# Kernel tuning notes

Hardware: AMD Instinct MI355X
Metric: run time of the kernel (lower is better)

## Reference

```python
import jax, jax.numpy as jnp
import numpy as np

B, S, H, F, E, K = 4, 2048, 512, 2048, 8, 2


def setup_inputs() -> dict:
    key = jax.random.key(0)
    ks = jax.random.split(key, 6)
    s_h = 1.0 / np.sqrt(H)
    s_f = 1.0 / np.sqrt(F)
    return {
        "x": jax.random.normal(ks[0], (B, S, H), dtype=jnp.float32),
        "router_w": jax.random.uniform(ks[1], (E, H), jnp.float32, -s_h, s_h),
        "fc1_w": jax.random.uniform(ks[2], (E, F, H), jnp.float32, -s_h, s_h),
        "fc1_b": jax.random.uniform(ks[3], (E, F), jnp.float32, -s_h, s_h),
        "fc2_w": jax.random.uniform(ks[4], (E, H, F), jnp.float32, -s_f, s_f),
        "fc2_b": jax.random.uniform(ks[5], (E, H), jnp.float32, -s_f, s_f),
    }


def reference(x, router_w, fc1_w, fc1_b, fc2_w, fc2_b):
    # Router: Linear (no bias), softmax over experts, top-k, renormalize.
    logits = jnp.einsum("bsh,eh->bse", x, router_w)           # [B,S,E]
    probs = jax.nn.softmax(logits, axis=-1)                    # [B,S,E]
    topk_p, topk_i = jax.lax.top_k(probs, K)                   # [B,S,K]
    topk_p = topk_p / (jnp.sum(topk_p, axis=-1, keepdims=True) + 1e-9)

    # Original loop runs every expert FFN on all tokens and masks;
    # mathematically identical: dense per-expert FFN, then gather+combine.
    h1 = jnp.einsum("bsh,efh->bsef", x, fc1_w) + fc1_b         # [B,S,E,F]
    a = jax.nn.gelu(h1, approximate=False)                     # exact erf GELU (torch nn.GELU default)
    y = jnp.einsum("bsef,ehf->bseh", a, fc2_w) + fc2_b         # [B,S,E,H]

    sel = jnp.take_along_axis(y, topk_i[..., None], axis=2)    # [B,S,K,H]
    output = jnp.sum(topk_p[..., None] * sel, axis=2)          # [B,S,H]
    return output, probs, topk_i
```

## Files before the change

### kernel.cpp

```cpp
#include <hip/hip_runtime.h>

#define T_TOKENS 8192
#define HD 512
#define FD 2048
#define NE 8
#define CAP 8192
#define CSTRIDE 32

#define BM 128
#define BN 128
#define BK 32

typedef __attribute__((ext_vector_type(8))) short short8;
typedef __attribute__((ext_vector_type(4))) float f32x4;

__device__ __forceinline__ ushort f2bf(float f) {
  union { float f; unsigned u; } v; v.f = f;
  unsigned u = v.u;
  return (ushort)((u + 0x7fffu + ((u >> 16) & 1u)) >> 16);
}

__device__ __forceinline__ void gld16(const void* g, void* l) {
  __builtin_amdgcn_global_load_lds(
      (const __attribute__((address_space(1))) void*)g,
      (__attribute__((address_space(3))) void*)l, 16, 0, 0);
}

__global__ void cvt_bf16(const float4* __restrict__ src, ushort4* __restrict__ dst, int n4) {
  int i = blockIdx.x * blockDim.x + threadIdx.x;
  int st = gridDim.x * blockDim.x;
  for (; i < n4; i += st) {
    float4 v = src[i];
    ushort4 o;
    o.x = f2bf(v.x); o.y = f2bf(v.y); o.z = f2bf(v.z); o.w = f2bf(v.w);
    dst[i] = o;
  }
}

#define TPW 16
__global__ void router_kernel(const float* __restrict__ x, const float* __restrict__ rw,
                              float* __restrict__ probs_out, float* __restrict__ topk_out,
                              int* __restrict__ counts, int* __restrict__ bucket_tok,
                              float* __restrict__ bucket_w, int4* __restrict__ tok_info) {
  __shared__ int lcnt[NE];
  __shared__ int lbase[NE];
  __shared__ int ls_e0[64], ls_e1[64], ls_s0[64], ls_s1[64];
  __shared__ float ls_w0[64], ls_w1[64];

  int wave = threadIdx.x >> 6, lane = threadIdx.x & 63;
  if (threadIdx.x < NE) lcnt[threadIdx.x] = 0;
  __syncthreads();

  int tbase = blockIdx.x * 64;
  for (int it = 0; it < TPW; it++) {
    int lt = wave * TPW + it;
    int t = tbase + lt;
    float acc[NE];
#pragma unroll
    for (int e = 0; e < NE; e++) acc[e] = 0.f;
    const float* xr = x + (size_t)t * HD;
    for (int c = 0; c < HD; c += 64) {
      float xv = xr[c + lane];
#pragma unroll
      for (int e = 0; e < NE; e++) acc[e] += xv * rw[e * HD + c + lane];
    }
#pragma unroll
    for (int e = 0; e < NE; e++) {
#pragma unroll
      for (int s = 32; s > 0; s >>= 1) acc[e] += __shfl_xor(acc[e], s, 64);
    }
    if (lane == 0) {
      float m = acc[0];
#pragma unroll
      for (int e = 1; e < NE; e++) m = fmaxf(m, acc[e]);
      float p[NE], s = 0.f;
#pragma unroll
      for (int e = 0; e < NE; e++) { p[e] = expf(acc[e] - m); s += p[e]; }
      float inv = 1.f / s;
#pragma unroll
      for (int e = 0; e < NE; e++) { p[e] *= inv; probs_out[(size_t)t * NE + e] = p[e]; }
      int i0 = 0;
#pragma unroll
      for (int e = 1; e < NE; e++) if (p[e] > p[i0]) i0 = e;
      int i1 = (i0 == 0) ? 1 : 0;
#pragma unroll
      for (int e = 0; e < NE; e++) if (e != i0 && p[e] > p[i1]) i1 = e;
      float r = 1.f / (p[i0] + p[i1] + 1e-9f);
      topk_out[(size_t)t * 2 + 0] = (float)i0;
      topk_out[(size_t)t * 2 + 1] = (float)i1;
      ls_e0[lt] = i0; ls_e1[lt] = i1;
      ls_w0[lt] = p[i0] * r; ls_w1[lt] = p[i1] * r;
      ls_s0[lt] = atomicAdd(&lcnt[i0], 1);
      ls_s1[lt] = atomicAdd(&lcnt[i1], 1);
    }
  }
  __syncthreads();
  if (threadIdx.x < NE)
    lbase[threadIdx.x] = atomicAdd(&counts[threadIdx.x * CSTRIDE], lcnt[threadIdx.x]);
  __syncthreads();
  if (threadIdx.x < 64) {
    int lt = threadIdx.x, t = tbase + lt;
    int e0 = ls_e0[lt], e1 = ls_e1[lt];
    int g0 = lbase[e0] + ls_s0[lt];
    int g1 = lbase[e1] + ls_s1[lt];
    bucket_tok[e0 * CAP + g0] = t; bucket_w[e0 * CAP + g0] = ls_w0[lt];
    bucket_tok[e1 * CAP + g1] = t; bucket_w[e1 * CAP + g1] = ls_w1[lt];
    tok_info[t] = make_int4(e0, e1, g0, g1);
  }
}

__global__ void scan_kernel(const int* __restrict__ counts, int* __restrict__ offsets) {
  if (threadIdx.x == 0) {
    int o = 0;
#pragma unroll
    for (int e = 0; e < NE; e++) { offsets[e] = o; o += counts[e * CSTRIDE]; }
  }
}

template <bool IS_FC1>
__global__ __launch_bounds__(256, 2)
void ffn_gemm(const ushort* __restrict__ Ab, const ushort* __restrict__ Bw,
              const float* __restrict__ bias, const int* __restrict__ counts,
              const int* __restrict__ offsets, const int* __restrict__ bucket_tok,
              const float* __restrict__ bucket_w, ushort* __restrict__ Aout,
              float* __restrict__ Yout, int KD, int ND) {
  int e = blockIdx.z;
  int cnt = counts[e * CSTRIDE];
  int m0 = blockIdx.y * BM;
  if (m0 >= cnt) return;
  int n0 = blockIdx.x * BN;
  int off = offsets[e];

  __shared__ alignas(16) ushort smem[10240];
  ushort* As = smem;
  ushort* Bs = smem + BM * BK;

  int tid = threadIdx.x;
  int wid = tid >> 6, lid = tid & 63;
  int wm = wid >> 1, wn = wid & 1;
  int q = lid >> 4, l16 = lid & 15;

  int crow = tid >> 2;
  int cseg = (tid & 3) * 8;

  int mr0 = min(m0 + crow, cnt - 1);
  int mr1 = min(m0 + crow + 64, cnt - 1);
  const ushort *a0, *a1;
  if (IS_FC1) {
    a0 = Ab + (size_t)bucket_tok[e * CAP + mr0] * KD + cseg;
    a1 = Ab + (size_t)bucket_tok[e * CAP + mr1] * KD + cseg;
  } else {
    a0 = Ab + (size_t)(off + mr0) * KD + cseg;
    a1 = Ab + (size_t)(off + mr1) * KD + cseg;
  }
  const ushort* b0 = Bw + ((size_t)e * ND + n0 + crow) * KD + cseg;
  const ushort* b1 = b0 + (size_t)64 * KD;
  ushort* lA0 = As + tid * 8;
  ushort* lA1 = As + (tid + 256) * 8;
  ushort* lB0 = Bs + tid * 8;
  ushort* lB1 = Bs + (tid + 256) * 8;

  f32x4 acc[4][4] = {};

  for (int k0 = 0; k0 < KD; k0 += BK) {
    gld16(a0 + k0, lA0);
    gld16(a1 + k0, lA1);
    gld16(b0 + k0, lB0);
    gld16(b1 + k0, lB1);
    __syncthreads();
    short8 af[4], bfr[4];
#pragma unroll
    for (int i = 0; i < 4; i++)
      af[i] = *(const short8*)&As[(wm * 64 + i * 16 + l16) * BK + q * 8];
#pragma unroll
    for (int j = 0; j < 4; j++)
      bfr[j] = *(const short8*)&Bs[(wn * 64 + j * 16 + l16) * BK + q * 8];
#pragma unroll
    for (int i = 0; i < 4; i++)
#pragma unroll
      for (int j = 0; j < 4; j++)
        acc[i][j] = __builtin_amdgcn_mfma_f32_16x16x32_bf16(af[i], bfr[j], acc[i][j], 0, 0, 0);
    __syncthreads();
  }

  float bcol[4];
#pragma unroll
  for (int j = 0; j < 4; j++)
    bcol[j] = bias[(size_t)e * ND + n0 + wn * 64 + j * 16 + l16];

  if (IS_FC1) {
    ushort* Ct = smem;
#pragma unroll
    for (int i = 0; i < 4; i++) {
      __syncthreads();
#pragma unroll
      for (int j = 0; j < 4; j++)
#pragma unroll
        for (int r = 0; r < 4; r++) {
          float v = acc[i][j][r] + bcol[j];
          float g = 0.5f * v * (1.0f + erff(v * 0.70710678118654752f));
          Ct[(wm * 16 + q * 4 + r) * 136 + wn * 64 + j * 16 + l16] = f2bf(g);
        }
      __syncthreads();
#pragma unroll
      for (int u = 0; u < 2; u++) {
        int c = tid + u * 256;
        int ml = c >> 4, cc = c & 15;
        int gm = m0 + (ml >> 4) * 64 + i * 16 + (ml & 15);
        if (gm < cnt)
          *(uint4*)&Aout[(size_t)(off + gm) * ND + n0 + cc * 8] =
              *(const uint4*)&Ct[ml * 136 + cc * 8];
      }
    }
  } else {
    float* Ct = (float*)smem;
#pragma unroll
    for (int i = 0; i < 4; i++) {
      __syncthreads();
#pragma unroll
      for (int r = 0; r < 4; r++) {
        int gm = m0 + wm * 64 + i * 16 + q * 4 + r;
        float wgt = bucket_w[e * CAP + min(gm, cnt - 1)];
#pragma unroll
        for (int j = 0; j < 4; j++)
          Ct[(wm * 16 + q * 4 + r) * 132 + wn * 64 + j * 16 + l16] = wgt * (acc[i][j][r] + bcol[j]);
      }
      __syncthreads();
#pragma unroll
      for (int u = 0; u < 4; u++) {
        int c = tid + u * 256;
        int ml = c >> 5, cc = c & 31;
        int gm = m0 + (ml >> 4) * 64 + i * 16 + (ml & 15);
        if (gm < cnt)
          *(float4*)&Yout[(size_t)(off + gm) * ND + n0 + cc * 4] =
              *(const float4*)&Ct[ml * 132 + cc * 4];
      }
    }
  }
}

__global__ void combine_kernel(const float4* __restrict__ Y, const int4* __restrict__ tok_info,
                               const int* __restrict__ offsets, float4* __restrict__ out) {
  int t = blockIdx.x;
  int4 ti = tok_info[t];
  int g0 = offsets[ti.x] + ti.z;
  int g1 = offsets[ti.y] + ti.w;
  int i = threadIdx.x;
  float4 a = Y[(size_t)g0 * (HD / 4) + i];
  float4 b = Y[(size_t)g1 * (HD / 4) + i];
  out[(size_t)t * (HD / 4) + i] = make_float4(a.x + b.x, a.y + b.y, a.z + b.z, a.w + b.w);
}

extern "C" void kernel_launch(void* const* d_in, const int* in_sizes, int n_in,
                              void* d_out, int out_size, void* d_ws, size_t ws_size,
                              hipStream_t stream) {
  const float* x    = (const float*)d_in[0];
  const float* rw   = (const float*)d_in[1];
  const float* fc1w = (const float*)d_in[2];
  const float* fc1b = (const float*)d_in[3];
  const float* fc2w = (const float*)d_in[4];
  const float* fc2b = (const float*)d_in[5];

  float* out   = (float*)d_out;
  float* probs = out + (size_t)T_TOKENS * HD;
  float* topk  = probs + (size_t)T_TOKENS * NE;

  char* p = (char*)d_ws;
  auto carve = [&](size_t bytes) { char* r = p; p += (bytes + 255) & ~(size_t)255; return r; };
  int*    counts     = (int*)carve(NE * CSTRIDE * sizeof(int));
  int*    offsets    = (int*)carve(NE * sizeof(int));
  int*    bucket_tok = (int*)carve((size_t)NE * CAP * sizeof(int));
  float*  bucket_w   = (float*)carve((size_t)NE * CAP * sizeof(float));
  int4*   tok_info   = (int4*)carve((size_t)T_TOKENS * sizeof(int4));
  ushort* xb   = (ushort*)carve((size_t)T_TOKENS * HD * 2);
  ushort* w1b  = (ushort*)carve((size_t)NE * FD * HD * 2);
  ushort* w2b  = (ushort*)carve((size_t)NE * HD * FD * 2);
  ushort* Abuf = (ushort*)carve((size_t)T_TOKENS * 2 * FD * 2);
  float*  Y    = (float*)carve((size_t)T_TOKENS * 2 * HD * 4);

  hipMemsetAsync(counts, 0, NE * CSTRIDE * sizeof(int), stream);
  cvt_bf16<<<2048, 256, 0, stream>>>((const float4*)x, (ushort4*)xb, T_TOKENS * HD / 4);
  cvt_bf16<<<2048, 256, 0, stream>>>((const float4*)fc1w, (ushort4*)w1b, NE * FD * HD / 4);
  cvt_bf16<<<2048, 256, 0, stream>>>((const float4*)fc2w, (ushort4*)w2b, NE * HD * FD / 4);
  router_kernel<<<T_TOKENS / 64, 256, 0, stream>>>(x, rw, probs, topk, counts, bucket_tok,
                                                   bucket_w, tok_info);
  scan_kernel<<<1, 64, 0, stream>>>(counts, offsets);
  ffn_gemm<true><<<dim3(FD / BN, CAP / BM, NE), 256, 0, stream>>>(
      xb, w1b, fc1b, counts, offsets, bucket_tok, bucket_w, Abuf, nullptr, HD, FD);
  ffn_gemm<false><<<dim3(HD / BN, CAP / BM, NE), 256, 0, stream>>>(
      Abuf, w2b, fc2b, counts, offsets, bucket_tok, bucket_w, nullptr, Y, FD, HD);
  combine_kernel<<<T_TOKENS, 128, 0, stream>>>((const float4*)Y, tok_info, offsets, (float4*)out);
}
```

Baseline: 339.1 us.

## Fuse fp32-to-bf16 weight conversion into FFN GEMM tile loads

```diff
diff --git a/kernel.cpp b/kernel.cpp
--- a/kernel.cpp
+++ b/kernel.cpp
@@ -8,8 +8,6 @@
 #define CSTRIDE 32
 
 #define BM 128
-#define BN 128
-#define BK 32
 
 typedef __attribute__((ext_vector_type(8))) short short8;
 typedef __attribute__((ext_vector_type(4))) float f32x4;
@@ -20,10 +18,9 @@
   return (ushort)((u + 0x7fffu + ((u >> 16) & 1u)) >> 16);
 }
 
-__device__ __forceinline__ void gld16(const void* g, void* l) {
-  __builtin_amdgcn_global_load_lds(
-      (const __attribute__((address_space(1))) void*)g,
-      (__attribute__((address_space(3))) void*)l, 16, 0, 0);
+__device__ __forceinline__ unsigned pack_trunc(float lo, float hi) {
+  union { float f; unsigned u; } a, b; a.f = lo; b.f = hi;
+  return __builtin_amdgcn_perm(b.u, a.u, 0x07060302);
 }
 
 __global__ void cvt_bf16(const float4* __restrict__ src, ushort4* __restrict__ dst, int n4) {
@@ -117,84 +114,112 @@
   }
 }
 
-template <bool IS_FC1>
+template <int BN_, bool IS_FC1>
 __global__ __launch_bounds__(256, 2)
-void ffn_gemm(const ushort* __restrict__ Ab, const ushort* __restrict__ Bw,
+void ffn_gemm(const ushort* __restrict__ Ab, const float* __restrict__ Bw,
               const float* __restrict__ bias, const int* __restrict__ counts,
               const int* __restrict__ offsets, const int* __restrict__ bucket_tok,
               const float* __restrict__ bucket_w, ushort* __restrict__ Aout,
               float* __restrict__ Yout, int KD, int ND) {
+  constexpr int JW = BN_ / 32;
+  constexpr int BCH_PT = BN_ / 32;
+
   int e = blockIdx.z;
   int cnt = counts[e * CSTRIDE];
   int m0 = blockIdx.y * BM;
   if (m0 >= cnt) return;
-  int n0 = blockIdx.x * BN;
+  int n0 = blockIdx.x * BN_;
   int off = offsets[e];
 
-  __shared__ alignas(16) ushort smem[10240];
-  ushort* As = smem;
-  ushort* Bs = smem + BM * BK;
+  __shared__ alignas(16) ushort As[8 * BM * 8];
+  __shared__ alignas(16) ushort Bs[8 * BN_ * 8];
 
   int tid = threadIdx.x;
   int wid = tid >> 6, lid = tid & 63;
   int wm = wid >> 1, wn = wid & 1;
   int q = lid >> 4, l16 = lid & 15;
 
-  int crow = tid >> 2;
-  int cseg = (tid & 3) * 8;
-
-  int mr0 = min(m0 + crow, cnt - 1);
-  int mr1 = min(m0 + crow + 64, cnt - 1);
-  const ushort *a0, *a1;
+  int kc = tid & 7;
+  int rbase = tid >> 3;
+
+  const ushort* aptr[4];
+  int aoff[4];
+#pragma unroll
+  for (int u = 0; u < 4; u++) {
+    int m = rbase + u * 32;
+    int mr = min(m0 + m, cnt - 1);
+    int row = IS_FC1 ? bucket_tok[e * CAP + mr] : (off + mr);
+    aptr[u] = Ab + (size_t)row * KD + kc * 8;
+    aoff[u] = (kc * BM + (m ^ kc)) * 8;
+  }
+  const float* bptr[BCH_PT];
+  int boff[BCH_PT];
+#pragma unroll
+  for (int u = 0; u < BCH_PT; u++) {
+    int n = rbase + u * 32;
+    bptr[u] = Bw + ((size_t)e * ND + n0 + n) * KD + kc * 8;
+    boff[u] = (kc * BN_ + (n ^ kc)) * 8;
+  }
+
+  f32x4 acc[4][JW] = {};
+
+  for (int k0 = 0; k0 < KD; k0 += 64) {
+    uint4 av[4];
+#pragma unroll
+    for (int u = 0; u < 4; u++) av[u] = *(const uint4*)(aptr[u] + k0);
+    float4 bv0[BCH_PT], bv1[BCH_PT];
+#pragma unroll
+    for (int u = 0; u < BCH_PT; u++) {
+      bv0[u] = *(const float4*)(bptr[u] + k0);
+      bv1[u] = *(const float4*)(bptr[u] + k0 + 4);
+    }
+#pragma unroll
+    for (int u = 0; u < 4; u++) *(uint4*)&As[aoff[u]] = av[u];
+#pragma unroll
+    for (int u = 0; u < BCH_PT; u++) {
+      uint4 o;
+      o.x = pack_trunc(bv0[u].x, bv0[u].y);
+      o.y = pack_trunc(bv0[u].z, bv0[u].w);
+      o.z = pack_trunc(bv1[u].x, bv1[u].y);
+      o.w = pack_trunc(bv1[u].z, bv1[u].w);
+      *(uint4*)&Bs[boff[u]] = o;
+    }
+    __syncthreads();
+#pragma unroll
+    for (int t = 0; t < 2; t++) {
+      int kcc = t * 4 + q;
+      short8 af[4], bfr[JW];
+#pragma unroll
+      for (int i = 0; i < 4; i++) {
+        int m = wm * 64 + i * 16 + l16;
+        af[i] = *(const short8*)&As[((kcc * BM) + (m ^ kcc)) * 8];
+      }
+#pragma unroll
+      for (int j = 0; j < JW; j++) {
+        int n = wn * (16 * JW) + j * 16 + l16;
+        bfr[j] = *(const short8*)&Bs[((kcc * BN_) + (n ^ kcc)) * 8];
+      }
+#pragma unroll
+      for (int i = 0; i < 4; i++)
+#pragma unroll
+        for (int j = 0; j < JW; j++)
+          acc[i][j] = __builtin_amdgcn_mfma_f32_16x16x32_bf16(af[i], bfr[j], acc[i][j], 0, 0, 0);
+    }
+    __syncthreads();
+  }
+
+  float bcol[JW];
+#pragma unroll
+  for (int j = 0; j < JW; j++)
+    bcol[j] = bias[(size_t)e * ND + n0 + wn * (16 * JW) + j * 16 + l16];
+
   if (IS_FC1) {
-    a0 = Ab + (size_t)bucket_tok[e * CAP + mr0] * KD + cseg;
-    a1 = Ab + (size_t)bucket_tok[e * CAP + mr1] * KD + cseg;
-  } else {
-    a0 = Ab + (size_t)(off + mr0) * KD + cseg;
-    a1 = Ab + (size_t)(off + mr1) * KD + cseg;
-  }
-  const ushort* b0 = Bw + ((size_t)e * ND + n0 + crow) * KD + cseg;
-  const ushort* b1 = b0 + (size_t)64 * KD;
-  ushort* lA0 = As + tid * 8;
-  ushort* lA1 = As + (tid + 256) * 8;
-  ushort* lB0 = Bs + tid * 8;
-  ushort* lB1 = Bs + (tid + 256) * 8;
-
-  f32x4 acc[4][4] = {};
-
-  for (int k0 = 0; k0 < KD; k0 += BK) {
-    gld16(a0 + k0, lA0);
-    gld16(a1 + k0, lA1);
-    gld16(b0 + k0, lB0);
-    gld16(b1 + k0, lB1);
-    __syncthreads();
-    short8 af[4], bfr[4];
-#pragma unroll
-    for (int i = 0; i < 4; i++)
-      af[i] = *(const short8*)&As[(wm * 64 + i * 16 + l16) * BK + q * 8];
-#pragma unroll
-    for (int j = 0; j < 4; j++)
-      bfr[j] = *(const short8*)&Bs[(wn * 64 + j * 16 + l16) * BK + q * 8];
-#pragma unroll
-    for (int i = 0; i < 4; i++)
-#pragma unroll
-      for (int j = 0; j < 4; j++)
-        acc[i][j] = __builtin_amdgcn_mfma_f32_16x16x32_bf16(af[i], bfr[j], acc[i][j], 0, 0, 0);
-    __syncthreads();
-  }
-
-  float bcol[4];
-#pragma unroll
-  for (int j = 0; j < 4; j++)
-    bcol[j] = bias[(size_t)e * ND + n0 + wn * 64 + j * 16 + l16];
-
-  if (IS_FC1) {
-    ushort* Ct = smem;
+    ushort* Ct = As;
 #pragma unroll
     for (int i = 0; i < 4; i++) {
       __syncthreads();
 #pragma unroll
-      for (int j = 0; j < 4; j++)
+      for (int j = 0; j < JW; j++)
 #pragma unroll
         for (int r = 0; r < 4; r++) {
           float v = acc[i][j][r] + bcol[j];
@@ -213,7 +238,7 @@
       }
     }
   } else {
-    float* Ct = (float*)smem;
+    float* Ct = (float*)As;
 #pragma unroll
     for (int i = 0; i < 4; i++) {
       __syncthreads();
@@ -222,18 +247,18 @@
         int gm = m0 + wm * 64 + i * 16 + q * 4 + r;
         float wgt = bucket_w[e * CAP + min(gm, cnt - 1)];
 #pragma unroll
-        for (int j = 0; j < 4; j++)
-          Ct[(wm * 16 + q * 4 + r) * 132 + wn * 64 + j * 16 + l16] = wgt * (acc[i][j][r] + bcol[j]);
+        for (int j = 0; j < JW; j++)
+          Ct[(wm * 16 + q * 4 + r) * 68 + wn * 32 + j * 16 + l16] = wgt * (acc[i][j][r] + bcol[j]);
       }
       __syncthreads();
 #pragma unroll
-      for (int u = 0; u < 4; u++) {
+      for (int u = 0; u < 2; u++) {
         int c = tid + u * 256;
-        int ml = c >> 5, cc = c & 31;
+        int ml = c >> 4, cc = c & 15;
         int gm = m0 + (ml >> 4) * 64 + i * 16 + (ml & 15);
         if (gm < cnt)
           *(float4*)&Yout[(size_t)(off + gm) * ND + n0 + cc * 4] =
-              *(const float4*)&Ct[ml * 132 + cc * 4];
+              *(const float4*)&Ct[ml * 68 + cc * 4];
       }
     }
   }
@@ -273,21 +298,17 @@
   float*  bucket_w   = (float*)carve((size_t)NE * CAP * sizeof(float));
   int4*   tok_info   = (int4*)carve((size_t)T_TOKENS * sizeof(int4));
   ushort* xb   = (ushort*)carve((size_t)T_TOKENS * HD * 2);
-  ushort* w1b  = (ushort*)carve((size_t)NE * FD * HD * 2);
-  ushort* w2b  = (ushort*)carve((size_t)NE * HD * FD * 2);
   ushort* Abuf = (ushort*)carve((size_t)T_TOKENS * 2 * FD * 2);
   float*  Y    = (float*)carve((size_t)T_TOKENS * 2 * HD * 4);
 
   hipMemsetAsync(counts, 0, NE * CSTRIDE * sizeof(int), stream);
   cvt_bf16<<<2048, 256, 0, stream>>>((const float4*)x, (ushort4*)xb, T_TOKENS * HD / 4);
-  cvt_bf16<<<2048, 256, 0, stream>>>((const float4*)fc1w, (ushort4*)w1b, NE * FD * HD / 4);
-  cvt_bf16<<<2048, 256, 0, stream>>>((const float4*)fc2w, (ushort4*)w2b, NE * HD * FD / 4);
   router_kernel<<<T_TOKENS / 64, 256, 0, stream>>>(x, rw, probs, topk, counts, bucket_tok,
                                                    bucket_w, tok_info);
   scan_kernel<<<1, 64, 0, stream>>>(counts, offsets);
-  ffn_gemm<true><<<dim3(FD / BN, CAP / BM, NE), 256, 0, stream>>>(
-      xb, w1b, fc1b, counts, offsets, bucket_tok, bucket_w, Abuf, nullptr, HD, FD);
-  ffn_gemm<false><<<dim3(HD / BN, CAP / BM, NE), 256, 0, stream>>>(
-      Abuf, w2b, fc2b, counts, offsets, bucket_tok, bucket_w, nullptr, Y, FD, HD);
+  ffn_gemm<128, true><<<dim3(FD / 128, CAP / BM, NE), 256, 0, stream>>>(
+      xb, fc1w, fc1b, counts, offsets, bucket_tok, bucket_w, Abuf, nullptr, HD, FD);
+  ffn_gemm<64, false><<<dim3(HD / 64, CAP / BM, NE), 256, 0, stream>>>(
+      Abuf, fc2w, fc2b, counts, offsets, bucket_tok, bucket_w, nullptr, Y, FD, HD);
   combine_kernel<<<T_TOKENS, 128, 0, stream>>>((const float4*)Y, tok_info, offsets, (float4*)out);
 }
```

After: 351.2 us. 3.6% more time.

## Double-buffer LDS tiles with k-chunk-major layout in expert GEMM

Applied to the files above, without the earlier changes.

```diff
diff --git a/kernel.cpp b/kernel.cpp
--- a/kernel.cpp
+++ b/kernel.cpp
@@ -118,7 +118,7 @@
 }
 
 template <bool IS_FC1>
-__global__ __launch_bounds__(256, 2)
+__global__ __launch_bounds__(256, 3)
 void ffn_gemm(const ushort* __restrict__ Ab, const ushort* __restrict__ Bw,
               const float* __restrict__ bias, const int* __restrict__ counts,
               const int* __restrict__ offsets, const int* __restrict__ bucket_tok,
@@ -131,56 +131,59 @@
   int n0 = blockIdx.x * BN;
   int off = offsets[e];
 
-  __shared__ alignas(16) ushort smem[10240];
-  ushort* As = smem;
-  ushort* Bs = smem + BM * BK;
+  __shared__ alignas(16) ushort smem[16384];
 
   int tid = threadIdx.x;
-  int wid = tid >> 6, lid = tid & 63;
+  int wid = tid >> 6, lane = tid & 63;
   int wm = wid >> 1, wn = wid & 1;
-  int q = lid >> 4, l16 = lid & 15;
-
-  int crow = tid >> 2;
-  int cseg = (tid & 3) * 8;
-
-  int mr0 = min(m0 + crow, cnt - 1);
-  int mr1 = min(m0 + crow + 64, cnt - 1);
-  const ushort *a0, *a1;
-  if (IS_FC1) {
-    a0 = Ab + (size_t)bucket_tok[e * CAP + mr0] * KD + cseg;
-    a1 = Ab + (size_t)bucket_tok[e * CAP + mr1] * KD + cseg;
-  } else {
-    a0 = Ab + (size_t)(off + mr0) * KD + cseg;
-    a1 = Ab + (size_t)(off + mr1) * KD + cseg;
-  }
-  const ushort* b0 = Bw + ((size_t)e * ND + n0 + crow) * KD + cseg;
-  const ushort* b1 = b0 + (size_t)64 * KD;
-  ushort* lA0 = As + tid * 8;
-  ushort* lA1 = As + (tid + 256) * 8;
-  ushort* lB0 = Bs + tid * 8;
-  ushort* lB1 = Bs + (tid + 256) * 8;
+  int q = lane >> 4, l16 = lane & 15;
+
+  int srow = tid & 127;
+  int kc0 = tid >> 7;
+  int mr = min(m0 + srow, cnt - 1);
+  int arow = IS_FC1 ? bucket_tok[e * CAP + mr] : (off + mr);
+  const ushort* ag = Ab + (size_t)arow * KD + kc0 * 8;
+  const ushort* bg = Bw + ((size_t)e * ND + n0 + srow) * KD + kc0 * 8;
 
   f32x4 acc[4][4] = {};
-
-  for (int k0 = 0; k0 < KD; k0 += BK) {
-    gld16(a0 + k0, lA0);
-    gld16(a1 + k0, lA1);
-    gld16(b0 + k0, lB0);
-    gld16(b1 + k0, lB1);
-    __syncthreads();
+  const int nIter = KD / BK;
+
+  {
+    ushort* al = smem + (size_t)tid * 8;
+    ushort* bl = smem + 4096 + (size_t)tid * 8;
+    gld16(ag, al);      gld16(ag + 16, al + 2048);
+    gld16(bg, bl);      gld16(bg + 16, bl + 2048);
+  }
+
+  for (int k = 0; k < nIter; k++) {
+    int pr = k & 1;
+    if (k + 1 < nIter) {
+      int pw = pr ^ 1;
+      const ushort* agn = ag + (size_t)(k + 1) * BK;
+      const ushort* bgn = bg + (size_t)(k + 1) * BK;
+      ushort* aln = smem + pw * 8192 + (size_t)tid * 8;
+      ushort* bln = smem + pw * 8192 + 4096 + (size_t)tid * 8;
+      gld16(agn, aln);      gld16(agn + 16, aln + 2048);
+      gld16(bgn, bln);      gld16(bgn + 16, bln + 2048);
+      asm volatile("s_waitcnt vmcnt(4)\ns_barrier" ::: "memory");
+    } else {
+      asm volatile("s_waitcnt vmcnt(0)\ns_barrier" ::: "memory");
+    }
+    const ushort* Ak = smem + pr * 8192;
+    const ushort* Bk = Ak + 4096;
     short8 af[4], bfr[4];
 #pragma unroll
     for (int i = 0; i < 4; i++)
-      af[i] = *(const short8*)&As[(wm * 64 + i * 16 + l16) * BK + q * 8];
+      af[i] = *(const short8*)&Ak[(q * BM + wm * 64 + i * 16 + l16) * 8];
 #pragma unroll
     for (int j = 0; j < 4; j++)
-      bfr[j] = *(const short8*)&Bs[(wn * 64 + j * 16 + l16) * BK + q * 8];
+      bfr[j] = *(const short8*)&Bk[(q * BN + wn * 64 + j * 16 + l16) * 8];
 #pragma unroll
     for (int i = 0; i < 4; i++)
 #pragma unroll
       for (int j = 0; j < 4; j++)
         acc[i][j] = __builtin_amdgcn_mfma_f32_16x16x32_bf16(af[i], bfr[j], acc[i][j], 0, 0, 0);
-    __syncthreads();
+    asm volatile("s_barrier" ::: "memory");
   }
 
   float bcol[4];
```

Result: slower. 415.3 us (+22.5%).
